# Performance work log

Measured on AMD Instinct MI355X. Metric: run time of the kernel, lower is better.

Reference implementation:

```python
import jax, jax.numpy as jnp
import numpy as np

N_HEAD = 16
N_KV_HEAD = 4
HEAD_DIM = 64
VE_CH = 12  # min(12, n_embd)


def apply_rotary_emb(x, cos, sin):
    d = x.shape[3] // 2
    x1, x2 = x[..., :d], x[..., d:]
    return jnp.concatenate([x1 * cos + x2 * sin, x1 * -sin + x2 * cos], axis=3)


def rms_norm(x):
    return x * jax.lax.rsqrt(jnp.mean(jnp.square(x), axis=-1, keepdims=True) + 1e-6)


def setup_inputs() -> dict:
    key = jax.random.key(0)
    ks = jax.random.split(key, 9)
    B, T, C = 2, 2048, 1024
    s = 0.02
    return {
        "x": jax.random.normal(ks[0], (B, T, C), jnp.float32),
        "ve": jax.random.normal(ks[1], (B, T, N_KV_HEAD * HEAD_DIM), jnp.float32),
        "cos": jax.random.normal(ks[2], (1, T, 1, HEAD_DIM // 2), jnp.float32),
        "sin": jax.random.normal(ks[3], (1, T, 1, HEAD_DIM // 2), jnp.float32),
        "Wq": jax.random.normal(ks[4], (C, C), jnp.float32) * s,
        "Wk": jax.random.normal(ks[5], (N_KV_HEAD * HEAD_DIM, C), jnp.float32) * s,
        "Wv": jax.random.normal(ks[6], (N_KV_HEAD * HEAD_DIM, C), jnp.float32) * s,
        "Wo": jax.random.normal(ks[7], (C, C), jnp.float32) * s,
        "Wg": jax.random.normal(ks[8], (N_KV_HEAD, VE_CH), jnp.float32) * s,
    }


def reference(x, ve, cos, sin, Wq, Wk, Wv, Wo, Wg):
    B, T, C = x.shape
    q = (x @ Wq.T).reshape(B, T, N_HEAD, HEAD_DIM)
    k = (x @ Wk.T).reshape(B, T, N_KV_HEAD, HEAD_DIM)
    v = (x @ Wv.T).reshape(B, T, N_KV_HEAD, HEAD_DIM)

    # value-embedding gate
    ve_r = ve.reshape(B, T, N_KV_HEAD, HEAD_DIM)
    gate = 3.0 * jax.nn.sigmoid(x[..., :VE_CH] @ Wg.T)  # [B,T,n_kv_head]
    v = v + gate[..., None] * ve_r

    q = apply_rotary_emb(q, cos, sin)
    k = apply_rotary_emb(k, cos, sin)
    q = rms_norm(q) * 1.2
    k = rms_norm(k) * 1.2

    # GQA: expand kv heads
    r = N_HEAD // N_KV_HEAD
    k = jnp.repeat(k, r, axis=2)
    v = jnp.repeat(v, r, axis=2)

    # [B,H,T,D]
    q = q.transpose(0, 2, 1, 3)
    k = k.transpose(0, 2, 1, 3)
    v = v.transpose(0, 2, 1, 3)

    scale = 1.0 / np.sqrt(HEAD_DIM).astype(np.float32)
    scores = jnp.einsum("bhqd,bhkd->bhqk", q, k) * scale
    causal = jnp.tril(jnp.ones((T, T), dtype=bool))
    scores = jnp.where(causal, scores, jnp.float32(-jnp.inf))
    att = jax.nn.softmax(scores, axis=-1)
    y = jnp.einsum("bhqk,bhkd->bhqd", att, v)
    y = y.transpose(0, 2, 1, 3).reshape(B, T, C)
    return y @ Wo.T
```

## Files before the change

kernel.cpp:

```cpp
#include <hip/hip_runtime.h>
#include <stdint.h>

#define B_SZ 2
#define T_SZ 2048
#define C_SZ 1024
#define NH   16
#define NKV  4
#define HD   64
#define KVD  256
#define QKV_N 1536

typedef __attribute__((ext_vector_type(8))) short bf16x8;
typedef __attribute__((ext_vector_type(4))) float f32x4;

#define GL(p) ((const __attribute__((address_space(1))) void*)(p))
#define LD(p) ((__attribute__((address_space(3))) void*)(p))

__device__ inline unsigned short f2bf(float f) {
  union { float f; unsigned u; } v; v.f = f;
  unsigned u = v.u;
  unsigned r = (u + 0x7fffu + ((u >> 16) & 1u)) >> 16;
  return (unsigned short)r;
}
__device__ inline unsigned short bftrunc(float f) {
  union { float f; unsigned u; } v; v.f = f;
  return (unsigned short)(v.u >> 16);
}

struct CvtArgs {
  const float *s0, *s1, *s2, *s3, *s4;
  unsigned short *d0, *d1, *d2, *d3, *d4;
  const float *x, *Wg;
  float *gate;
};
__global__ __launch_bounds__(256) void cvt_all(CvtArgs a) {
  int blk = blockIdx.x, tid = threadIdx.x;
  if (blk >= 6656) {
    int idx = (blk - 6656) * 256 + tid;
    int bt = idx >> 2, kh = idx & 3;
    float s = 0.f;
#pragma unroll
    for (int j = 0; j < 12; j++) s += a.x[(size_t)bt * C_SZ + j] * a.Wg[kh * 12 + j];
    a.gate[idx] = 3.f / (1.f + __expf(-s));
    return;
  }
  const float* s; unsigned short* d; int i;
  if      (blk < 4096) { s = a.s0; d = a.d0; i = blk * 256 + tid; }
  else if (blk < 5120) { s = a.s1; d = a.d1; i = (blk - 4096) * 256 + tid; }
  else if (blk < 5376) { s = a.s2; d = a.d2; i = (blk - 5120) * 256 + tid; }
  else if (blk < 5632) { s = a.s3; d = a.d3; i = (blk - 5376) * 256 + tid; }
  else                 { s = a.s4; d = a.d4; i = (blk - 5632) * 256 + tid; }
  float4 f = ((const float4*)s)[i];
  ushort4 o;
  o.x = f2bf(f.x); o.y = f2bf(f.y); o.z = f2bf(f.z); o.w = f2bf(f.w);
  ((ushort4*)d)[i] = o;
}

#define GEMM_PROLOG(A, Bm, K)                                                        \
  __shared__ unsigned short As[2][64 * 64];                                          \
  __shared__ unsigned short Bs[2][128 * 64];                                         \
  int tid  = threadIdx.x;                                                            \
  int lane = tid & 63;                                                               \
  int wave = tid >> 6;                                                               \
  int quad = lane >> 4;                                                              \
  int l16  = lane & 15;                                                              \
  int m0 = blockIdx.y * 64;                                                          \
  int n0 = blockIdx.x * 128;                                                         \
  int wm = (wave & 1) * 32;                                                          \
  int wn = (wave >> 1) * 64;                                                         \
  f32x4 acc[2][4];                                                                   \
  _Pragma("unroll") for (int i = 0; i < 2; i++)                                      \
    _Pragma("unroll") for (int j = 0; j < 4; j++)                                    \
      acc[i][j] = (f32x4){0.f, 0.f, 0.f, 0.f};                                       \
  int lrow = lane >> 3;                                 \
  int lcol = ((lane & 7) ^ lrow) * 8;                 \
  int sA = wave * 16;                                                                \
  int sB = wave * 32;                                                                \
  const unsigned short* aP0 = &A[(size_t)(m0 + sA + lrow) * K + lcol];               \
  const unsigned short* aP1 = aP0 + 8 * (size_t)K;                                   \
  const unsigned short* bP0 = &Bm[(size_t)(n0 + sB + lrow) * K + lcol];              \
  const unsigned short* bP1 = bP0 + 8 * (size_t)K;                                   \
  const unsigned short* bP2 = bP0 + 16 * (size_t)K;                                  \
  const unsigned short* bP3 = bP0 + 24 * (size_t)K;                                  \
  __builtin_amdgcn_global_load_lds(GL(aP0), LD(&As[0][(sA     ) * 64]), 16, 0, 0);   \
  __builtin_amdgcn_global_load_lds(GL(aP1), LD(&As[0][(sA +  8) * 64]), 16, 0, 0);   \
  __builtin_amdgcn_global_load_lds(GL(bP0), LD(&Bs[0][(sB     ) * 64]), 16, 0, 0);   \
  __builtin_amdgcn_global_load_lds(GL(bP1), LD(&Bs[0][(sB +  8) * 64]), 16, 0, 0);   \
  __builtin_amdgcn_global_load_lds(GL(bP2), LD(&Bs[0][(sB + 16) * 64]), 16, 0, 0);   \
  __builtin_amdgcn_global_load_lds(GL(bP3), LD(&Bs[0][(sB + 24) * 64]), 16, 0, 0);   \
  int swz = l16 & 7;                                                                 \
  int nk = K >> 6;                                                                   \
  for (int ki = 0; ki < nk; ki++) {                                                  \
    int cur = ki & 1, nxt = cur ^ 1;                                                 \
    __syncthreads();                                                                 \
    if (ki + 1 < nk) {                                                               \
      int k0 = (ki + 1) << 6;                                                        \
      __builtin_amdgcn_global_load_lds(GL(aP0 + k0), LD(&As[nxt][(sA     ) * 64]), 16, 0, 0); \
      __builtin_amdgcn_global_load_lds(GL(aP1 + k0), LD(&As[nxt][(sA +  8) * 64]), 16, 0, 0); \
      __builtin_amdgcn_global_load_lds(GL(bP0 + k0), LD(&Bs[nxt][(sB     ) * 64]), 16, 0, 0); \
      __builtin_amdgcn_global_load_lds(GL(bP1 + k0), LD(&Bs[nxt][(sB +  8) * 64]), 16, 0, 0); \
      __builtin_amdgcn_global_load_lds(GL(bP2 + k0), LD(&Bs[nxt][(sB + 16) * 64]), 16, 0, 0); \
      __builtin_amdgcn_global_load_lds(GL(bP3 + k0), LD(&Bs[nxt][(sB + 24) * 64]), 16, 0, 0); \
    }                                                                                \
    _Pragma("unroll") for (int p = 0; p < 2; p++) {                                  \
      bf16x8 af[2], bfr[4];                                                          \
      _Pragma("unroll") for (int i = 0; i < 2; i++)                                  \
        af[i] = *(const bf16x8*)&As[cur][(wm + i * 16 + l16) * 64 + (((p * 4 + quad) ^ swz) * 8)]; \
      _Pragma("unroll") for (int j = 0; j < 4; j++)                                  \
        bfr[j] = *(const bf16x8*)&Bs[cur][(wn + j * 16 + l16) * 64 + (((p * 4 + quad) ^ swz) * 8)]; \
      _Pragma("unroll") for (int i = 0; i < 2; i++)                                  \
        _Pragma("unroll") for (int j = 0; j < 4; j++)                                \
          acc[i][j] = __builtin_amdgcn_mfma_f32_16x16x32_bf16(af[i], bfr[j], acc[i][j], 0, 0, 0); \
    }                                                                                \
  }

__global__ __launch_bounds__(256) void gemm_bt(const unsigned short* __restrict__ A,
                                               const unsigned short* __restrict__ Bm,
                                               float* __restrict__ C,
                                               int N, int K) {
  GEMM_PROLOG(A, Bm, K)
#pragma unroll
  for (int i = 0; i < 2; i++) {
#pragma unroll
    for (int j = 0; j < 4; j++) {
      int col = n0 + wn + j * 16 + l16;
#pragma unroll
      for (int r = 0; r < 4; r++) {
        int row = m0 + wm + i * 16 + quad * 4 + r;
        C[(size_t)row * N + col] = acc[i][j][r];
      }
    }
  }
}

__global__ __launch_bounds__(256) void gemm_qkv(const unsigned short* __restrict__ A,
                                                const unsigned short* __restrict__ Bm,
                                                const float* __restrict__ ve,
                                                const float* __restrict__ cosb,
                                                const float* __restrict__ sinb,
                                                const float* __restrict__ gateArr,
                                                unsigned short* __restrict__ qa,
                                                unsigned short* __restrict__ ka,
                                                unsigned short* __restrict__ vtmp) {
  const int K = C_SZ;
  GEMM_PROLOG(A, Bm, K)

  int colbase = n0 + wn;
  if (colbase < 1280) {
    int isQ = colbase < 1024;
    int h   = isQ ? (colbase >> 6) : ((colbase - 1024) >> 6);
    float scale = isQ ? (0.15f * 1.44269504088896f) : 1.2f;
    unsigned short* dst = isQ ? qa : ka;
    int nheads = isQ ? NH : NKV;
#pragma unroll
    for (int i = 0; i < 2; i++) {
#pragma unroll
      for (int r = 0; r < 4; r++) {
        int row = m0 + wm + i * 16 + quad * 4 + r;
        int t = row & (T_SZ - 1), b = row >> 11;
        float a10 = acc[i][0][r], a11 = acc[i][1][r];
        float a20 = acc[i][2][r], a21 = acc[i][3][r];
        float cv0 = cosb[t * 32 + l16],      sv0 = sinb[t * 32 + l16];
        float cv1 = cosb[t * 32 + 16 + l16], sv1 = sinb[t * 32 + 16 + l16];
        float o10 =  a10 * cv0 + a20 * sv0;
        float o11 =  a11 * cv1 + a21 * sv1;
        float o20 = -a10 * sv0 + a20 * cv0;
        float o21 = -a11 * sv1 + a21 * cv1;
        float ssq = o10 * o10 + o11 * o11 + o20 * o20 + o21 * o21;
        ssq += __shfl_xor(ssq, 1);
        ssq += __shfl_xor(ssq, 2);
        ssq += __shfl_xor(ssq, 4);
        ssq += __shfl_xor(ssq, 8);
        float rn = rsqrtf(ssq * (1.f / 64.f) + 1e-6f) * scale;
        size_t base = ((size_t)(b * nheads + h) * T_SZ + t) * HD;
        dst[base + l16]      = f2bf(o10 * rn);
        dst[base + 16 + l16] = f2bf(o11 * rn);
        dst[base + 32 + l16] = f2bf(o20 * rn);
        dst[base + 48 + l16] = f2bf(o21 * rn);
      }
    }
  } else {
    int kh = (colbase - 1280) >> 6;
#pragma unroll
    for (int i = 0; i < 2; i++) {
#pragma unroll
      for (int r = 0; r < 4; r++) {
        int row = m0 + wm + i * 16 + quad * 4 + r;
        float g = gateArr[row * 4 + kh];
#pragma unroll
        for (int j = 0; j < 4; j++) {
          int d = j * 16 + l16;
          float val = acc[i][j][r] + g * ve[(size_t)row * KVD + kh * HD + d];
          vtmp[(size_t)row * KVD + kh * HD + d] = f2bf(val);
        }
      }
    }
  }
}

__global__ __launch_bounds__(256) void v_transpose(const unsigned short* __restrict__ vtmp,
                                                   unsigned short* __restrict__ vt) {
  __shared__ unsigned short tile[64 * 68];
  int blk = blockIdx.x;
  int tb = blk & 31, kh = (blk >> 5) & 3, b = blk >> 7;
  int tid = threadIdx.x;
  int r = tid >> 2, c = (tid & 3) * 16;
  const unsigned short* src = &vtmp[((size_t)(b * T_SZ + tb * 64 + r)) * KVD + kh * HD + c];
  uint4 x0 = *(const uint4*)(src);
  uint4 x1 = *(const uint4*)(src + 8);
  *(uint2*)&tile[r * 68 + c]      = *(uint2*)&x0;
  *(uint2*)&tile[r * 68 + c + 4]  = *((uint2*)&x0 + 1);
  *(uint2*)&tile[r * 68 + c + 8]  = *(uint2*)&x1;
  *(uint2*)&tile[r * 68 + c + 12] = *((uint2*)&x1 + 1);
  __syncthreads();
  int d = tid >> 2, tc = (tid & 3) * 16;
  ushort4 o0, o1, o2, o3;
  o0.x = tile[(tc + 0) * 68 + d];  o0.y = tile[(tc + 1) * 68 + d];
  o0.z = tile[(tc + 2) * 68 + d];  o0.w = tile[(tc + 3) * 68 + d];
  o1.x = tile[(tc + 4) * 68 + d];  o1.y = tile[(tc + 5) * 68 + d];
  o1.z = tile[(tc + 6) * 68 + d];  o1.w = tile[(tc + 7) * 68 + d];
  o2.x = tile[(tc + 8) * 68 + d];  o2.y = tile[(tc + 9) * 68 + d];
  o2.z = tile[(tc + 10) * 68 + d]; o2.w = tile[(tc + 11) * 68 + d];
  o3.x = tile[(tc + 12) * 68 + d]; o3.y = tile[(tc + 13) * 68 + d];
  o3.z = tile[(tc + 14) * 68 + d]; o3.w = tile[(tc + 15) * 68 + d];
  unsigned short* dst = &vt[((size_t)(b * NKV + kh) * HD + d) * T_SZ + tb * 64 + tc];
  *(ushort4*)(dst)      = o0;
  *(ushort4*)(dst + 4)  = o1;
  *(ushort4*)(dst + 8)  = o2;
  *(ushort4*)(dst + 12) = o3;
}

#define KST 72
#define PST 72
__global__ __launch_bounds__(256) void attn(const unsigned short* __restrict__ qa,
                                            const unsigned short* __restrict__ ka,
                                            const unsigned short* __restrict__ vt,
                                            unsigned short* __restrict__ y) {
  int bid = blockIdx.x;
  int half = bid >> 8, r = bid & 255;
  int qt = half ? (r & 15) : 15 - (r & 15);
  int bh = (half << 4) | (r >> 4);
  int b = bh >> 4, h = bh & 15;
  int kh = h >> 2;
  int tid = threadIdx.x;
  int wave = tid >> 6, lane = tid & 63;
  int quad = lane >> 4, l16 = lane & 15;

  __shared__ unsigned short Ks[2][64 * KST];
  __shared__ unsigned short Vs[2][64 * KST];
  __shared__ unsigned short Ps[128 * PST];
  unsigned short* Pw = &Ps[(wave * 32) * PST];

  bf16x8 bq[2][2];
#pragma unroll
  for (int qi = 0; qi < 2; qi++) {
    int tq = qt * 128 + wave * 32 + qi * 16 + l16;
    const unsigned short* qp = &qa[((size_t)(b * NH + h) * T_SZ + tq) * HD];
    bq[qi][0] = *(const bf16x8*)&qp[quad * 8];
    bq[qi][1] = *(const bf16x8*)&qp[32 + quad * 8];
  }

  const unsigned short one_bf = 0x3F80;
  bf16x8 vones = {(short)one_bf, (short)one_bf, (short)one_bf, (short)one_bf,
                  (short)one_bf, (short)one_bf, (short)one_bf, (short)one_bf};

  f32x4 oacc[2][4];
  f32x4 lacc[2];
#pragma unroll
  for (int qi = 0; qi < 2; qi++) {
    lacc[qi] = (f32x4){0.f, 0.f, 0.f, 0.f};
#pragma unroll
    for (int d = 0; d < 4; d++) oacc[qi][d] = (f32x4){0.f, 0.f, 0.f, 0.f};
  }

  int lr = tid >> 2;
  int lc = (tid & 3) * 16;

  const unsigned short* kbase = &ka[(size_t)(b * NKV + kh) * T_SZ * HD];
  const unsigned short* vbase = &vt[(size_t)(b * NKV + kh) * HD * T_SZ];

  int nj = 2 * qt + 2;

  {
    const unsigned short* kp = &kbase[(size_t)lr * HD + lc];
    const unsigned short* vp = &vbase[(size_t)lr * T_SZ + lc];
    uint4 k0 = *(const uint4*)(kp);
    uint4 k1 = *(const uint4*)(kp + 8);
    uint4 v0 = *(const uint4*)(vp);
    uint4 v1 = *(const uint4*)(vp + 8);
    *(uint4*)&Ks[0][lr * KST + lc]     = k0;
    *(uint4*)&Ks[0][lr * KST + lc + 8] = k1;
    *(uint4*)&Vs[0][lr * KST + lc]     = v0;
    *(uint4*)&Vs[0][lr * KST + lc + 8] = v1;
  }

  int qrow0 = qt * 128 + wave * 32;

  for (int j = 0; j < nj; j++) {
    int cur = j & 1, nxt = cur ^ 1;
    __syncthreads();

    uint4 k0, k1, v0, v1;
    bool pf = (j + 1 < nj);
    if (pf) {
      const unsigned short* kp = &kbase[(size_t)((j + 1) * 64 + lr) * HD + lc];
      const unsigned short* vp = &vbase[(size_t)lr * T_SZ + (j + 1) * 64 + lc];
      k0 = *(const uint4*)(kp);
      k1 = *(const uint4*)(kp + 8);
      v0 = *(const uint4*)(vp);
      v1 = *(const uint4*)(vp + 8);
    }

    f32x4 st[4][2];
#pragma unroll
    for (int tb = 0; tb < 4; tb++) {
      bf16x8 ak0 = *(const bf16x8*)&Ks[cur][(tb * 16 + l16) * KST + quad * 8];
      bf16x8 ak1 = *(const bf16x8*)&Ks[cur][(tb * 16 + l16) * KST + 32 + quad * 8];
#pragma unroll
      for (int qi = 0; qi < 2; qi++) {
        f32x4 s = (f32x4){0.f, 0.f, 0.f, 0.f};
        s = __builtin_amdgcn_mfma_f32_16x16x32_bf16(ak0, bq[qi][0], s, 0, 0, 0);
        s = __builtin_amdgcn_mfma_f32_16x16x32_bf16(ak1, bq[qi][1], s, 0, 0, 0);
        st[tb][qi] = s;
      }
    }

#pragma unroll
    for (int qi = 0; qi < 2; qi++) {
      int qlow = qrow0 + qi * 16;
      if (j * 64 + 63 > qlow) {
        int qg = qlow + l16;
#pragma unroll
        for (int tb = 0; tb < 4; tb++) {
          int tg = j * 64 + tb * 16 + quad * 4;
#pragma unroll
          for (int i = 0; i < 4; i++) {
            if (tg + i > qg) st[tb][qi][i] = -__builtin_inff();
          }
        }
      }
#pragma unroll
      for (int tb = 0; tb < 4; tb++) {
        ushort4 w;
        w.x = bftrunc(__builtin_amdgcn_exp2f(st[tb][qi][0]));
        w.y = bftrunc(__builtin_amdgcn_exp2f(st[tb][qi][1]));
        w.z = bftrunc(__builtin_amdgcn_exp2f(st[tb][qi][2]));
        w.w = bftrunc(__builtin_amdgcn_exp2f(st[tb][qi][3]));
        *(ushort4*)&Pw[(qi * 16 + l16) * PST + tb * 16 + quad * 4] = w;
      }
    }

    bf16x8 ap[2][2];
#pragma unroll
    for (int qi = 0; qi < 2; qi++) {
      ap[qi][0] = *(const bf16x8*)&Pw[(qi * 16 + l16) * PST + quad * 8];
      ap[qi][1] = *(const bf16x8*)&Pw[(qi * 16 + l16) * PST + 32 + quad * 8];
      lacc[qi] = __builtin_amdgcn_mfma_f32_16x16x32_bf16(ap[qi][0], vones, lacc[qi], 0, 0, 0);
      lacc[qi] = __builtin_amdgcn_mfma_f32_16x16x32_bf16(ap[qi][1], vones, lacc[qi], 0, 0, 0);
    }
#pragma unroll
    for (int d = 0; d < 4; d++) {
      bf16x8 bv0 = *(const bf16x8*)&Vs[cur][(d * 16 + l16) * KST + quad * 8];
      bf16x8 bv1 = *(const bf16x8*)&Vs[cur][(d * 16 + l16) * KST + 32 + quad * 8];
#pragma unroll
      for (int qi = 0; qi < 2; qi++) {
        oacc[qi][d] = __builtin_amdgcn_mfma_f32_16x16x32_bf16(ap[qi][0], bv0, oacc[qi][d], 0, 0, 0);
        oacc[qi][d] = __builtin_amdgcn_mfma_f32_16x16x32_bf16(ap[qi][1], bv1, oacc[qi][d], 0, 0, 0);
      }
    }

    if (pf) {
      *(uint4*)&Ks[nxt][lr * KST + lc]     = k0;
      *(uint4*)&Ks[nxt][lr * KST + lc + 8] = k1;
      *(uint4*)&Vs[nxt][lr * KST + lc]     = v0;
      *(uint4*)&Vs[nxt][lr * KST + lc + 8] = v1;
    }
  }

#pragma unroll
  for (int qi = 0; qi < 2; qi++) {
#pragma unroll
    for (int i = 0; i < 4; i++) {
      int tq = qrow0 + qi * 16 + quad * 4 + i;
      float inv = 1.f / lacc[qi][i];
#pragma unroll
      for (int d = 0; d < 4; d++) {
        y[((size_t)(b * T_SZ) + tq) * C_SZ + h * HD + d * 16 + l16] = f2bf(oacc[qi][d][i] * inv);
      }
    }
  }
}

extern "C" void kernel_launch(void* const* d_in, const int* in_sizes, int n_in,
                              void* d_out, int out_size, void* d_ws, size_t ws_size,
                              hipStream_t stream) {
  const float* x    = (const float*)d_in[0];
  const float* ve   = (const float*)d_in[1];
  const float* cosb = (const float*)d_in[2];
  const float* sinb = (const float*)d_in[3];
  const float* Wq   = (const float*)d_in[4];
  const float* Wk   = (const float*)d_in[5];
  const float* Wv   = (const float*)d_in[6];
  const float* Wo   = (const float*)d_in[7];
  const float* Wg   = (const float*)d_in[8];
  float* out = (float*)d_out;

  const size_t MB = 1024 * 1024;
  char* ws = (char*)d_ws;
  unsigned short* xb    = (unsigned short*)(ws);
  unsigned short* wqkvb = (unsigned short*)(ws + 8 * MB);
  unsigned short* wob   = (unsigned short*)(ws + 11 * MB);
  unsigned short* qab   = (unsigned short*)(ws + 13 * MB);
  unsigned short* kab   = (unsigned short*)(ws + 21 * MB);
  unsigned short* vtb   = (unsigned short*)(ws + 23 * MB);
  float*          gateA = (float*)(ws + 25 * MB);
  unsigned short* vtmp  = (unsigned short*)(ws + 26 * MB);
  unsigned short* yb    = xb;

  CvtArgs ca;
  ca.s0 = x;  ca.d0 = xb;
  ca.s1 = Wq; ca.d1 = wqkvb;
  ca.s2 = Wk; ca.d2 = wqkvb + 1024 * 1024;
  ca.s3 = Wv; ca.d3 = wqkvb + 1280 * 1024;
  ca.s4 = Wo; ca.d4 = wob;
  ca.x = x; ca.Wg = Wg; ca.gate = gateA;
  cvt_all<<<6720, 256, 0, stream>>>(ca);

  gemm_qkv<<<dim3(QKV_N / 128, (B_SZ * T_SZ) / 64), 256, 0, stream>>>(
      xb, wqkvb, ve, cosb, sinb, gateA, qab, kab, vtmp);

  v_transpose<<<256, 256, 0, stream>>>(vtmp, vtb);

  attn<<<512, 256, 0, stream>>>(qab, kab, vtb, yb);

  gemm_bt<<<dim3(C_SZ / 128, (B_SZ * T_SZ) / 64), 256, 0, stream>>>(
      yb, wob, out, C_SZ, C_SZ);
}
```

Measured before the change: 170.0 us.

## Split attention query tile across 8 waves with 16 rows each

The attention kernel now launches 512 threads (8 waves) per block instead of 4, and each wave owns 16 query rows instead of 32. K/V tile loads are spread over twice as many threads. Waves whose rows lie entirely before the current key block skip the QK/PV work for that block. The intent is more waves in flight to hide latency, fewer registers per wave, and less wasted work on causal diagonal blocks. In exchange, each K/V fragment read from shared memory is reused across fewer query rows, and barrier synchronization now spans more waves.

```diff
diff --git a/kernel.cpp b/kernel.cpp
--- a/kernel.cpp
+++ b/kernel.cpp
@@ -232,10 +232,10 @@
 
 #define KST 72
 #define PST 72
-__global__ __launch_bounds__(256) void attn(const unsigned short* __restrict__ qa,
-                                            const unsigned short* __restrict__ ka,
-                                            const unsigned short* __restrict__ vt,
-                                            unsigned short* __restrict__ y) {
+__global__ __launch_bounds__(512, 4) void attn(const unsigned short* __restrict__ qa,
+                                               const unsigned short* __restrict__ ka,
+                                               const unsigned short* __restrict__ vt,
+                                               unsigned short* __restrict__ y) {
   int bid = blockIdx.x;
   int half = bid >> 8, r = bid & 255;
   int qt = half ? (r & 15) : 15 - (r & 15);
@@ -249,32 +249,29 @@
   __shared__ unsigned short Ks[2][64 * KST];
   __shared__ unsigned short Vs[2][64 * KST];
   __shared__ unsigned short Ps[128 * PST];
-  unsigned short* Pw = &Ps[(wave * 32) * PST];
-
-  bf16x8 bq[2][2];
-#pragma unroll
-  for (int qi = 0; qi < 2; qi++) {
-    int tq = qt * 128 + wave * 32 + qi * 16 + l16;
+  unsigned short* Pw = &Ps[(wave * 16) * PST];
+
+  int qrow0 = qt * 128 + wave * 16;
+
+  bf16x8 bq0, bq1;
+  {
+    int tq = qrow0 + l16;
     const unsigned short* qp = &qa[((size_t)(b * NH + h) * T_SZ + tq) * HD];
-    bq[qi][0] = *(const bf16x8*)&qp[quad * 8];
-    bq[qi][1] = *(const bf16x8*)&qp[32 + quad * 8];
+    bq0 = *(const bf16x8*)&qp[quad * 8];
+    bq1 = *(const bf16x8*)&qp[32 + quad * 8];
   }
 
   const unsigned short one_bf = 0x3F80;
   bf16x8 vones = {(short)one_bf, (short)one_bf, (short)one_bf, (short)one_bf,
                   (short)one_bf, (short)one_bf, (short)one_bf, (short)one_bf};
 
-  f32x4 oacc[2][4];
-  f32x4 lacc[2];
-#pragma unroll
-  for (int qi = 0; qi < 2; qi++) {
-    lacc[qi] = (f32x4){0.f, 0.f, 0.f, 0.f};
-#pragma unroll
-    for (int d = 0; d < 4; d++) oacc[qi][d] = (f32x4){0.f, 0.f, 0.f, 0.f};
-  }
-
-  int lr = tid >> 2;
-  int lc = (tid & 3) * 16;
+  f32x4 oacc[4];
+  f32x4 lacc = (f32x4){0.f, 0.f, 0.f, 0.f};
+#pragma unroll
+  for (int d = 0; d < 4; d++) oacc[d] = (f32x4){0.f, 0.f, 0.f, 0.f};
+
+  int lr = tid >> 3;
+  int lc = (tid & 7) * 8;
 
   const unsigned short* kbase = &ka[(size_t)(b * NKV + kh) * T_SZ * HD];
   const unsigned short* vbase = &vt[(size_t)(b * NKV + kh) * HD * T_SZ];
@@ -285,108 +282,85 @@
     const unsigned short* kp = &kbase[(size_t)lr * HD + lc];
     const unsigned short* vp = &vbase[(size_t)lr * T_SZ + lc];
     uint4 k0 = *(const uint4*)(kp);
-    uint4 k1 = *(const uint4*)(kp + 8);
     uint4 v0 = *(const uint4*)(vp);
-    uint4 v1 = *(const uint4*)(vp + 8);
-    *(uint4*)&Ks[0][lr * KST + lc]     = k0;
-    *(uint4*)&Ks[0][lr * KST + lc + 8] = k1;
-    *(uint4*)&Vs[0][lr * KST + lc]     = v0;
-    *(uint4*)&Vs[0][lr * KST + lc + 8] = v1;
-  }
-
-  int qrow0 = qt * 128 + wave * 32;
+    *(uint4*)&Ks[0][lr * KST + lc] = k0;
+    *(uint4*)&Vs[0][lr * KST + lc] = v0;
+  }
 
   for (int j = 0; j < nj; j++) {
     int cur = j & 1, nxt = cur ^ 1;
     __syncthreads();
 
-    uint4 k0, k1, v0, v1;
+    uint4 k0, v0;
     bool pf = (j + 1 < nj);
     if (pf) {
       const unsigned short* kp = &kbase[(size_t)((j + 1) * 64 + lr) * HD + lc];
       const unsigned short* vp = &vbase[(size_t)lr * T_SZ + (j + 1) * 64 + lc];
       k0 = *(const uint4*)(kp);
-      k1 = *(const uint4*)(kp + 8);
       v0 = *(const uint4*)(vp);
-      v1 = *(const uint4*)(vp + 8);
-    }
-
-    f32x4 st[4][2];
-#pragma unroll
-    for (int tb = 0; tb < 4; tb++) {
-      bf16x8 ak0 = *(const bf16x8*)&Ks[cur][(tb * 16 + l16) * KST + quad * 8];
-      bf16x8 ak1 = *(const bf16x8*)&Ks[cur][(tb * 16 + l16) * KST + 32 + quad * 8];
-#pragma unroll
-      for (int qi = 0; qi < 2; qi++) {
+    }
+
+    bool active = (j * 64) <= (qrow0 + 15);
+
+    if (active) {
+      f32x4 st[4];
+#pragma unroll
+      for (int tb = 0; tb < 4; tb++) {
+        bf16x8 ak0 = *(const bf16x8*)&Ks[cur][(tb * 16 + l16) * KST + quad * 8];
+        bf16x8 ak1 = *(const bf16x8*)&Ks[cur][(tb * 16 + l16) * KST + 32 + quad * 8];
         f32x4 s = (f32x4){0.f, 0.f, 0.f, 0.f};
-        s = __builtin_amdgcn_mfma_f32_16x16x32_bf16(ak0, bq[qi][0], s, 0, 0, 0);
-        s = __builtin_amdgcn_mfma_f32_16x16x32_bf16(ak1, bq[qi][1], s, 0, 0, 0);
-        st[tb][qi] = s;
-      }
-    }
-
-#pragma unroll
-    for (int qi = 0; qi < 2; qi++) {
-      int qlow = qrow0 + qi * 16;
-      if (j * 64 + 63 > qlow) {
-        int qg = qlow + l16;
+        s = __builtin_amdgcn_mfma_f32_16x16x32_bf16(ak0, bq0, s, 0, 0, 0);
+        s = __builtin_amdgcn_mfma_f32_16x16x32_bf16(ak1, bq1, s, 0, 0, 0);
+        st[tb] = s;
+      }
+
+      if (j * 64 + 63 > qrow0) {
+        int qg = qrow0 + l16;
 #pragma unroll
         for (int tb = 0; tb < 4; tb++) {
           int tg = j * 64 + tb * 16 + quad * 4;
 #pragma unroll
           for (int i = 0; i < 4; i++) {
-            if (tg + i > qg) st[tb][qi][i] = -__builtin_inff();
+            if (tg + i > qg) st[tb][i] = -__builtin_inff();
           }
         }
       }
 #pragma unroll
       for (int tb = 0; tb < 4; tb++) {
         ushort4 w;
-        w.x = bftrunc(__builtin_amdgcn_exp2f(st[tb][qi][0]));
-        w.y = bftrunc(__builtin_amdgcn_exp2f(st[tb][qi][1]));
-        w.z = bftrunc(__builtin_amdgcn_exp2f(st[tb][qi][2]));
-        w.w = bftrunc(__builtin_amdgcn_exp2f(st[tb][qi][3]));
-        *(ushort4*)&Pw[(qi * 16 + l16) * PST + tb * 16 + quad * 4] = w;
-      }
-    }
-
-    bf16x8 ap[2][2];
-#pragma unroll
-    for (int qi = 0; qi < 2; qi++) {
-      ap[qi][0] = *(const bf16x8*)&Pw[(qi * 16 + l16) * PST + quad * 8];
-      ap[qi][1] = *(const bf16x8*)&Pw[(qi * 16 + l16) * PST + 32 + quad * 8];
-      lacc[qi] = __builtin_amdgcn_mfma_f32_16x16x32_bf16(ap[qi][0], vones, lacc[qi], 0, 0, 0);
-      lacc[qi] = __builtin_amdgcn_mfma_f32_16x16x32_bf16(ap[qi][1], vones, lacc[qi], 0, 0, 0);
-    }
+        w.x = bftrunc(__builtin_amdgcn_exp2f(st[tb][0]));
+        w.y = bftrunc(__builtin_amdgcn_exp2f(st[tb][1]));
+        w.z = bftrunc(__builtin_amdgcn_exp2f(st[tb][2]));
+        w.w = bftrunc(__builtin_amdgcn_exp2f(st[tb][3]));
+        *(ushort4*)&Pw[l16 * PST + tb * 16 + quad * 4] = w;
+      }
+
+      bf16x8 ap0 = *(const bf16x8*)&Pw[l16 * PST + quad * 8];
+      bf16x8 ap1 = *(const bf16x8*)&Pw[l16 * PST + 32 + quad * 8];
+      lacc = __builtin_amdgcn_mfma_f32_16x16x32_bf16(ap0, vones, lacc, 0, 0, 0);
+      lacc = __builtin_amdgcn_mfma_f32_16x16x32_bf16(ap1, vones, lacc, 0, 0, 0);
+#pragma unroll
+      for (int d = 0; d < 4; d++) {
+        bf16x8 bv0 = *(const bf16x8*)&Vs[cur][(d * 16 + l16) * KST + quad * 8];
+        bf16x8 bv1 = *(const bf16x8*)&Vs[cur][(d * 16 + l16) * KST + 32 + quad * 8];
+        oacc[d] = __builtin_amdgcn_mfma_f32_16x16x32_bf16(ap0, bv0, oacc[d], 0, 0, 0);
+        oacc[d] = __builtin_amdgcn_mfma_f32_16x16x32_bf16(ap1, bv1, oacc[d], 0, 0, 0);
+      }
+    }
+
+    if (pf) {
+      *(uint4*)&Ks[nxt][lr * KST + lc] = k0;
+      *(uint4*)&Vs[nxt][lr * KST + lc] = v0;
+    }
+  }
+
+#pragma unroll
+  for (int i = 0; i < 4; i++) {
+    int tq = qrow0 + quad * 4 + i;
+    float inv = 1.f / lacc[i];
 #pragma unroll
     for (int d = 0; d < 4; d++) {
-      bf16x8 bv0 = *(const bf16x8*)&Vs[cur][(d * 16 + l16) * KST + quad * 8];
-      bf16x8 bv1 = *(const bf16x8*)&Vs[cur][(d * 16 + l16) * KST + 32 + quad * 8];
-#pragma unroll
-      for (int qi = 0; qi < 2; qi++) {
-        oacc[qi][d] = __builtin_amdgcn_mfma_f32_16x16x32_bf16(ap[qi][0], bv0, oacc[qi][d], 0, 0, 0);
-        oacc[qi][d] = __builtin_amdgcn_mfma_f32_16x16x32_bf16(ap[qi][1], bv1, oacc[qi][d], 0, 0, 0);
-      }
-    }
-
-    if (pf) {
-      *(uint4*)&Ks[nxt][lr * KST + lc]     = k0;
-      *(uint4*)&Ks[nxt][lr * KST + lc + 8] = k1;
-      *(uint4*)&Vs[nxt][lr * KST + lc]     = v0;
-      *(uint4*)&Vs[nxt][lr * KST + lc + 8] = v1;
-    }
-  }
-
-#pragma unroll
-  for (int qi = 0; qi < 2; qi++) {
-#pragma unroll
-    for (int i = 0; i < 4; i++) {
-      int tq = qrow0 + qi * 16 + quad * 4 + i;
-      float inv = 1.f / lacc[qi][i];
-#pragma unroll
-      for (int d = 0; d < 4; d++) {
-        y[((size_t)(b * T_SZ) + tq) * C_SZ + h * HD + d * 16 + l16] = f2bf(oacc[qi][d][i] * inv);
-      }
+      y[((size_t)(b * T_SZ) + tq) * C_SZ + h * HD + d * 16 + l16] = f2bf(oacc[d][i] * inv);
     }
   }
 }
@@ -431,7 +405,7 @@
 
   v_transpose<<<256, 256, 0, stream>>>(vtmp, vtb);
 
-  attn<<<512, 256, 0, stream>>>(qab, kab, vtb, yb);
+  attn<<<512, 512, 0, stream>>>(qab, kab, vtb, yb);
 
   gemm_bt<<<dim3(C_SZ / 128, (B_SZ * T_SZ) / 64), 256, 0, stream>>>(
       yb, wob, out, C_SZ, C_SZ);
```

New measurement: 163.5 us. 3.9% less time.
